# Kernel optimization log

Measured on AMD Instinct MI355X. Metric: run time of the kernel, lower is better.

The kernel has to match this reference:

```python
import jax, jax.numpy as jnp
import numpy as np
from jax import lax

GAMMA = 0.99

def setup_inputs() -> dict:
    key = jax.random.key(0)
    ks = jax.random.split(key, 6)
    B, T, D = 2048, 512, 16
    return {
        "Q": jax.random.normal(ks[0], (B, T, D), dtype=jnp.float32),
        "expected_target_Q": jax.random.normal(ks[1], (B, T, D), dtype=jnp.float32),
        "target_Q": jax.random.normal(ks[2], (B, T, D), dtype=jnp.float32),
        "rewards": jax.random.normal(ks[3], (B, T, D), dtype=jnp.float32),
        "target_policy_probs": jax.random.normal(ks[4], (B, T, D), dtype=jnp.float32),
        "behaviour_policy_probs": jax.random.normal(ks[5], (B, T), dtype=jnp.float32),
    }


def _q_ret(expected_target_Q, target_Q, rewards, target_policy_probs, behaviour_policy_probs):
    # importance weights c = exp(min(log_pi - log_b, 0)), shape [B, T, D]
    c = jnp.exp(jnp.minimum(target_policy_probs - behaviour_policy_probs[..., None], 0.0))
    T = target_Q.shape[1]
    # time-major slices for steps j = 0..T-2
    tm = lambda x: jnp.swapaxes(x, 0, 1)  # [T, B, D] -> scan over leading axis
    xs = (tm(rewards[:, : T - 1]), tm(expected_target_Q[:, 1:]),
          tm(c[:, 1:]), tm(target_Q[:, 1:]))

    def step(carry, x):
        r, e, cw, tq = x
        q = r + GAMMA * (e + cw * (carry - tq))
        return q, q

    # reverse scan: Q_ret[j] depends on Q_ret[j+1]; init carry is target_Q[:, -1]
    _, q_ret = lax.scan(step, target_Q[:, -1], xs, reverse=True)
    return jnp.swapaxes(q_ret, 0, 1)  # [B, T-1, D] == Q_ret[:, :-1]


def reference(Q, expected_target_Q, target_Q, rewards, target_policy_probs, behaviour_policy_probs):
    q_ret = lax.stop_gradient(
        _q_ret(expected_target_Q, target_Q, rewards, target_policy_probs, behaviour_policy_probs))
    return jnp.mean((Q[:, :-1] - q_ret) ** 2)
```

## Files before the change

### kernel.cpp

```cpp
#include <hip/hip_runtime.h>


constexpr int B  = 2048;
constexpr int T  = 512;
constexpr int D  = 16;
constexpr int NC = 16;
constexpr int CS = 32;
constexpr int BPB = 4;
constexpr int ROWS = CS + 1;
constexpr int SQ = B * (D / 4);
constexpr float GAMMA = 0.99f;
constexpr float LOG2E = 1.44269504088896340736f;

constexpr int SEG = ROWS * D;
constexpr int ARR = BPB * SEG;
constexpr int LDS_FLOATS = 5 * ARR + BPB * ROWS;

__device__ __forceinline__ void load_lds16(const float* g, float* l) {
    __builtin_amdgcn_global_load_lds(
        (const __attribute__((address_space(1))) unsigned int*)g,
        (__attribute__((address_space(3))) unsigned int*)l, 16, 0, 0);
}
__device__ __forceinline__ void load_lds4(const float* g, float* l) {
    __builtin_amdgcn_global_load_lds(
        (const __attribute__((address_space(1))) unsigned int*)g,
        (__attribute__((address_space(3))) unsigned int*)l, 4, 0, 0);
}

__global__ __launch_bounds__(64) void retrace_phase1(
    const float* __restrict__ Q,
    const float* __restrict__ eQ,
    const float* __restrict__ tQ,
    const float* __restrict__ rw,
    const float* __restrict__ tpp,
    const float* __restrict__ bpp,
    float* __restrict__ ws)
{
    __shared__ float lds[LDS_FLOATS];

    const int tid = threadIdx.x;
    const int k   = blockIdx.y;
    const int b0  = blockIdx.x * BPB;
    const int t0  = k * CS;

    const bool last = (k == NC - 1);
    const int rows = last ? CS : ROWS;
    const int n4   = rows * D / 4;

    const float* gbase[5] = {Q, eQ, tQ, rw, tpp};
    #pragma unroll
    for (int a = 0; a < 5; ++a) {
        #pragma unroll
        for (int bl = 0; bl < BPB; ++bl) {
            const float* g = gbase[a] + ((size_t)(b0 + bl) * T + t0) * D;
            float* l = lds + a * ARR + bl * SEG;
            for (int off = tid; off < n4; off += 64)
                load_lds16(g + (size_t)off * 4, l + (size_t)off * 4);
        }
    }
    #pragma unroll
    for (int bl = 0; bl < BPB; ++bl) {
        const float* g = bpp + (size_t)(b0 + bl) * T + t0;
        float* l = lds + 5 * ARR + bl * ROWS;
        if (tid < rows) load_lds4(g + tid, l + tid);
    }
    __syncthreads();

    const int bl = tid >> 4;
    const int d  = tid & 15;
    const float* lQ = lds + 0 * ARR + bl * SEG + d;
    const float* lE = lds + 1 * ARR + bl * SEG + d;
    const float* lT = lds + 2 * ARR + bl * SEG + d;
    const float* lR = lds + 3 * ARR + bl * SEG + d;
    const float* lP = lds + 4 * ARR + bl * SEG + d;
    const float* lB = lds + 5 * ARR + bl * ROWS;

    const int steps = last ? (CS - 1) : CS;

    float alpha = 0.f, beta = 1.f, P = 0.f, S = 0.f, W = 0.f;
    #pragma unroll 8
    for (int i = steps - 1; i >= 0; --i) {
        const float tp = lP[(i + 1) * D];
        const float tq = lT[(i + 1) * D];
        const float ev = lE[(i + 1) * D];
        const float rv = lR[i * D];
        const float qv = lQ[i * D];
        const float bp = lB[i + 1];

        const float cw = __builtin_exp2f(fminf(tp - bp, 0.f) * LOG2E);
        const float g  = GAMMA * cw;
        const float base = fmaf(-g, tq, fmaf(GAMMA, ev, rv));
        alpha = fmaf(g, alpha, base);
        beta  = g * beta;
        const float u = qv - alpha;
        P = fmaf(u, u, P);
        S = fmaf(u, beta, S);
        W = fmaf(beta, beta, W);
    }

    const size_t AS = (size_t)NC * SQ * 4;
    const size_t o  = ((size_t)k * SQ + (size_t)b0 * 4) * 4 + tid;
    ws[0 * AS + o] = alpha;
    ws[1 * AS + o] = beta;
    ws[2 * AS + o] = P;
    ws[3 * AS + o] = S;
    ws[4 * AS + o] = W;
}

__global__ __launch_bounds__(64) void retrace_phase2(
    const float* __restrict__ tQ,
    const float4* __restrict__ ws,
    float* __restrict__ out)
{
    const int s  = blockIdx.x * blockDim.x + threadIdx.x;
    const int b  = s >> 2;
    const int dq = s & 3;

    const float4* wsA = ws;
    const float4* wsM = ws + (size_t)NC * SQ;
    const float4* wsP = ws + (size_t)2 * NC * SQ;
    const float4* wsS = ws + (size_t)3 * NC * SQ;
    const float4* wsW = ws + (size_t)4 * NC * SQ;

    float4 c4 = ((const float4*)tQ)[((size_t)b * T + (T - 1)) * 4 + dq];
    float* c = (float*)&c4;
    float loss[4] = {0.f, 0.f, 0.f, 0.f};

    #pragma unroll
    for (int k = NC - 1; k >= 0; --k) {
        const size_t o = (size_t)k * SQ + s;
        const float4 A4 = wsA[o], M4 = wsM[o], P4 = wsP[o], S4 = wsS[o], W4 = wsW[o];
        const float* A = (const float*)&A4;
        const float* M = (const float*)&M4;
        const float* P = (const float*)&P4;
        const float* S = (const float*)&S4;
        const float* W = (const float*)&W4;
        #pragma unroll
        for (int i = 0; i < 4; ++i) {
            loss[i] += fmaf(c[i], fmaf(W[i], c[i], -2.f * S[i]), P[i]);
            c[i] = fmaf(M[i], c[i], A[i]);
        }
    }

    float acc = (loss[0] + loss[1]) + (loss[2] + loss[3]);
    #pragma unroll
    for (int off = 32; off > 0; off >>= 1)
        acc += __shfl_down(acc, off, 64);

    if (threadIdx.x == 0) {
        constexpr float inv_count = 1.0f / ((float)B * (float)(T - 1) * (float)D);
        atomicAdd(out, acc * inv_count);
    }
}

extern "C" void kernel_launch(void* const* d_in, const int* in_sizes, int n_in,
                              void* d_out, int out_size, void* d_ws, size_t ws_size,
                              hipStream_t stream) {
    const float* Q   = (const float*)d_in[0];
    const float* eQ  = (const float*)d_in[1];
    const float* tQ  = (const float*)d_in[2];
    const float* rw  = (const float*)d_in[3];
    const float* tpp = (const float*)d_in[4];
    const float* bpp = (const float*)d_in[5];
    float* out = (float*)d_out;
    float* ws = (float*)d_ws;

    hipMemsetAsync(out, 0, sizeof(float), stream);

    retrace_phase1<<<dim3(B / BPB, NC), dim3(64), 0, stream>>>(
        Q, eQ, tQ, rw, tpp, bpp, ws);

    retrace_phase2<<<dim3(SQ / 64), dim3(64), 0, stream>>>(tQ, (const float4*)ws, out);
}
```

Before: 300.3 us.

## Precompute step coefficients in parallel before serial scan; load inputs via registers

Phase 1 now loads eQ, tQ, tpp, rewards and the behaviour probabilities into registers with coalesced float4 loads. All 64 threads compute the per-step coefficients (base and gamma*c, including the exp) in parallel and store them interleaved in LDS, so the serial reverse loop only reads a float2 plus Q. This takes the exp and the extra loads off the sequential dependency chain and cuts the LDS footprint. Only Q still uses direct global-to-LDS loads. It adds register pressure, and launch bounds now request two blocks per unit.

After: 305.1 us. No clear change (+1.6%).

```diff
diff --git a/kernel.cpp b/kernel.cpp
--- a/kernel.cpp
+++ b/kernel.cpp
@@ -7,27 +7,21 @@
 constexpr int NC = 16;
 constexpr int CS = 32;
 constexpr int BPB = 4;
-constexpr int ROWS = CS + 1;
 constexpr int SQ = B * (D / 4);
 constexpr float GAMMA = 0.99f;
 constexpr float LOG2E = 1.44269504088896340736f;
 
-constexpr int SEG = ROWS * D;
-constexpr int ARR = BPB * SEG;
-constexpr int LDS_FLOATS = 5 * ARR + BPB * ROWS;
+constexpr int QSEG  = CS * D + 16;
+constexpr int BGSEG = CS * D * 2 + 16;
+constexpr int LDS_FLOATS = BPB * QSEG + BPB * BGSEG;
 
 __device__ __forceinline__ void load_lds16(const float* g, float* l) {
     __builtin_amdgcn_global_load_lds(
         (const __attribute__((address_space(1))) unsigned int*)g,
         (__attribute__((address_space(3))) unsigned int*)l, 16, 0, 0);
 }
-__device__ __forceinline__ void load_lds4(const float* g, float* l) {
-    __builtin_amdgcn_global_load_lds(
-        (const __attribute__((address_space(1))) unsigned int*)g,
-        (__attribute__((address_space(3))) unsigned int*)l, 4, 0, 0);
-}
-
-__global__ __launch_bounds__(64) void retrace_phase1(
+
+__global__ __launch_bounds__(64, 2) void retrace_phase1(
     const float* __restrict__ Q,
     const float* __restrict__ eQ,
     const float* __restrict__ tQ,
@@ -36,7 +30,9 @@
     const float* __restrict__ bpp,
     float* __restrict__ ws)
 {
-    __shared__ float lds[LDS_FLOATS];
+    __shared__ __align__(16) float lds[LDS_FLOATS];
+    float* lQ  = lds;
+    float* lBG = lds + BPB * QSEG;
 
     const int tid = threadIdx.x;
     const int k   = blockIdx.y;
@@ -44,53 +40,84 @@
     const int t0  = k * CS;
 
     const bool last = (k == NC - 1);
-    const int rows = last ? CS : ROWS;
-    const int n4   = rows * D / 4;
-
-    const float* gbase[5] = {Q, eQ, tQ, rw, tpp};
-    #pragma unroll
-    for (int a = 0; a < 5; ++a) {
-        #pragma unroll
-        for (int bl = 0; bl < BPB; ++bl) {
-            const float* g = gbase[a] + ((size_t)(b0 + bl) * T + t0) * D;
-            float* l = lds + a * ARR + bl * SEG;
-            for (int off = tid; off < n4; off += 64)
-                load_lds16(g + (size_t)off * 4, l + (size_t)off * 4);
-        }
-    }
+    const int rows = last ? (CS - 1) : CS;
+    const int n4   = rows * (D / 4);
+
+    float4 ev4[BPB][2], tq4[BPB][2], tp4[BPB][2], rv4[BPB][2];
+    float  bpv[BPB][2];
     #pragma unroll
     for (int bl = 0; bl < BPB; ++bl) {
-        const float* g = bpp + (size_t)(b0 + bl) * T + t0;
-        float* l = lds + 5 * ARR + bl * ROWS;
-        if (tid < rows) load_lds4(g + tid, l + tid);
-    }
+        const size_t rb = ((size_t)(b0 + bl) * T + t0) * (D / 4);
+        const float4* ge = (const float4*)eQ  + rb + (D / 4);
+        const float4* gt = (const float4*)tQ  + rb + (D / 4);
+        const float4* gp = (const float4*)tpp + rb + (D / 4);
+        const float4* gr = (const float4*)rw  + rb;
+        const float*  gb = bpp + (size_t)(b0 + bl) * T + t0 + 1;
+        #pragma unroll
+        for (int h = 0; h < 2; ++h) {
+            const int off = tid + 64 * h;
+            if (off < n4) {
+                ev4[bl][h] = ge[off];
+                tq4[bl][h] = gt[off];
+                tp4[bl][h] = gp[off];
+                rv4[bl][h] = gr[off];
+                bpv[bl][h] = gb[off >> 2];
+            }
+        }
+    }
+
+    #pragma unroll
+    for (int bl = 0; bl < BPB; ++bl) {
+        const float* gq = Q + ((size_t)(b0 + bl) * T + t0) * D;
+        float* l = lQ + bl * QSEG;
+        #pragma unroll
+        for (int h = 0; h < 2; ++h) {
+            const int off = tid + 64 * h;
+            if (off < n4) load_lds16(gq + (size_t)off * 4, l + (size_t)off * 4);
+        }
+    }
+
+    #pragma unroll
+    for (int bl = 0; bl < BPB; ++bl) {
+        float* lbg = lBG + bl * BGSEG;
+        #pragma unroll
+        for (int h = 0; h < 2; ++h) {
+            const int off = tid + 64 * h;
+            if (off < n4) {
+                const float* e = (const float*)&ev4[bl][h];
+                const float* t = (const float*)&tq4[bl][h];
+                const float* p = (const float*)&tp4[bl][h];
+                const float* r = (const float*)&rv4[bl][h];
+                const float bp = bpv[bl][h];
+                float bg[8];
+                #pragma unroll
+                for (int j = 0; j < 4; ++j) {
+                    const float cw = __builtin_exp2f(fminf(p[j] - bp, 0.f) * LOG2E);
+                    const float g  = GAMMA * cw;
+                    bg[2 * j]     = fmaf(-g, t[j], fmaf(GAMMA, e[j], r[j]));
+                    bg[2 * j + 1] = g;
+                }
+                float4* dst = (float4*)(lbg + (size_t)off * 8);
+                dst[0] = make_float4(bg[0], bg[1], bg[2], bg[3]);
+                dst[1] = make_float4(bg[4], bg[5], bg[6], bg[7]);
+            }
+        }
+    }
+
     __syncthreads();
 
     const int bl = tid >> 4;
     const int d  = tid & 15;
-    const float* lQ = lds + 0 * ARR + bl * SEG + d;
-    const float* lE = lds + 1 * ARR + bl * SEG + d;
-    const float* lT = lds + 2 * ARR + bl * SEG + d;
-    const float* lR = lds + 3 * ARR + bl * SEG + d;
-    const float* lP = lds + 4 * ARR + bl * SEG + d;
-    const float* lB = lds + 5 * ARR + bl * ROWS;
-
-    const int steps = last ? (CS - 1) : CS;
+    const float* sQ  = lQ  + bl * QSEG + d;
+    const float* sBG = lBG + bl * BGSEG + 2 * d;
 
     float alpha = 0.f, beta = 1.f, P = 0.f, S = 0.f, W = 0.f;
     #pragma unroll 8
-    for (int i = steps - 1; i >= 0; --i) {
-        const float tp = lP[(i + 1) * D];
-        const float tq = lT[(i + 1) * D];
-        const float ev = lE[(i + 1) * D];
-        const float rv = lR[i * D];
-        const float qv = lQ[i * D];
-        const float bp = lB[i + 1];
-
-        const float cw = __builtin_exp2f(fminf(tp - bp, 0.f) * LOG2E);
-        const float g  = GAMMA * cw;
-        const float base = fmaf(-g, tq, fmaf(GAMMA, ev, rv));
-        alpha = fmaf(g, alpha, base);
+    for (int i = rows - 1; i >= 0; --i) {
+        const float2 bg = *(const float2*)(sBG + 32 * i);
+        const float qv  = sQ[i * D];
+        const float g   = bg.y;
+        alpha = fmaf(g, alpha, bg.x);
         beta  = g * beta;
         const float u = qv - alpha;
         P = fmaf(u, u, P);
```
